# Kernel tuning notes

Measured on AMD Instinct MI355X. Metric: run time of the kernel, lower is better.

## Reference

```python
import jax, jax.numpy as jnp
import numpy as np
from jax import lax

B, CIN, H, W = 32, 256, 56, 56
COUT, M, K = 256, 2, 3
CMID = COUT * M  # 512
SPARSITY = 0.9


def _make_binary_weight(key):
    k1, k2 = jax.random.split(key)
    shape = (CMID, CIN, K, K)
    mask = jax.random.bernoulli(k1, SPARSITY, shape)
    sign = jax.random.bernoulli(k2, 0.5, shape).astype(jnp.float32) * 2.0 - 1.0
    return jnp.where(mask, sign, 0.0).astype(jnp.float32)


def setup_inputs() -> dict:
    key = jax.random.key(0)
    kx, kw, kfw, kfb = jax.random.split(key, 4)
    x = jax.random.normal(kx, (B, CIN, H, W), dtype=jnp.float32)
    binary_w = _make_binary_weight(kw)
    fan_in = CMID  # 1x1 conv fan-in
    bound = 1.0 / np.sqrt(fan_in)
    fc_w = jax.random.uniform(kfw, (COUT, CMID, 1, 1), minval=-bound, maxval=bound, dtype=jnp.float32)
    fc_b = jax.random.uniform(kfb, (COUT,), minval=-bound, maxval=bound, dtype=jnp.float32)
    return {"x": x, "binary_w": binary_w, "fc_w": fc_w, "fc_b": fc_b}


def reference(x, binary_w, fc_w, fc_b):
    pad = K // 2
    # fixed random ternary conv, stride 1, same padding
    y = lax.conv_general_dilated(
        x, binary_w, window_strides=(1, 1), padding=[(pad, pad), (pad, pad)],
        dimension_numbers=("NCHW", "OIHW", "NCHW"))
    y = jax.nn.relu(y)
    # learnable 1x1 conv with bias
    y = lax.conv_general_dilated(
        y, fc_w, window_strides=(1, 1), padding=[(0, 0), (0, 0)],
        dimension_numbers=("NCHW", "OIHW", "NCHW"))
    return y + fc_b[None, :, None, None]
```

## Files before the change

kernel.cpp:

```cpp
#include <hip/hip_runtime.h>
#include <hip/hip_bf16.h>
#include <stdint.h>


typedef __attribute__((ext_vector_type(8))) short short8;
typedef __attribute__((ext_vector_type(4))) float floatx4;

#define ROWE 8192
#define NT_PER_B 28

#define OFF_WP  0
#define OFF_A2  2359296
#define OFF_XP  2621440
#define OFF_Y   63439872

__device__ static inline void async16(const void* gptr, void* lptr) {
  __builtin_amdgcn_global_load_lds(
      (const __attribute__((address_space(1))) void*)gptr,
      (__attribute__((address_space(3))) void*)lptr,
      16, 0, 0);
}

__device__ static inline unsigned short f2bf(float x) {
  __hip_bfloat16 h = __float2bfloat16(x);
  return *reinterpret_cast<unsigned short*>(&h);
}

__global__ void k_xprep(const float* __restrict__ x, __hip_bfloat16* __restrict__ Xp) {
  const int t = blockIdx.x * 256 + threadIdx.x;
  const int wq  = t & 63;
  const int khi = (t >> 6) & 15;
  const int t2  = t >> 10;
  const int hp  = t2 % 58;
  const int bc  = t2 / 58;
  const int b   = bc >> 1;
  const int cin0 = ((bc & 1) << 7) + (khi << 3);
  const int h = hp - 1, w = wq - 1;
  unsigned short v[8];
  if ((unsigned)h < 56u && (unsigned)w < 56u) {
    const float* xp = x + ((size_t)(b * 256 + cin0) * 56 + h) * 56 + w;
#pragma unroll
    for (int j = 0; j < 8; ++j) v[j] = f2bf(xp[(size_t)j * 3136]);
  } else {
#pragma unroll
    for (int j = 0; j < 8; ++j) v[j] = 0;
  }
  uint4 pk;
  pk.x = (unsigned)v[0] | ((unsigned)v[1] << 16);
  pk.y = (unsigned)v[2] | ((unsigned)v[3] << 16);
  pk.z = (unsigned)v[4] | ((unsigned)v[5] << 16);
  pk.w = (unsigned)v[6] | ((unsigned)v[7] << 16);
  *(uint4*)(Xp + (size_t)t * 8) = pk;
}

__global__ void k_wprep(const float* __restrict__ bw, __hip_bfloat16* __restrict__ Wp) {
  const int idx = blockIdx.x * 256 + threadIdx.x;
  const int klo = idx & 7;
  const int cml = (idx >> 3) & 63;
  const int khi = (idx >> 9) & 15;
  const int cmh = (idx >> 13) & 1;
  const int rest = idx >> 14;
  const int cmblk = rest & 3;
  const int tcg = rest >> 2;
  const int cg  = tcg & 1;
  const int tap = tcg >> 1;
  const int kh = tap / 3, kw = tap - kh * 3;
  const int cm  = (cmblk << 7) + (cmh << 6) + cml;
  const int cin = (cg << 7) + (khi << 3) + klo;
  Wp[idx] = __float2bfloat16(bw[((cm * 256 + cin) * 3 + kh) * 3 + kw]);
}

__global__ void k_a2prep(const float* __restrict__ fw, __hip_bfloat16* __restrict__ A2) {
  const int idx = blockIdx.x * 256 + threadIdx.x;
  const int klo = idx & 7;
  const int cl  = (idx >> 3) & 63;
  const int khi = (idx >> 9) & 15;
  const int ch  = (idx >> 13) & 1;
  const int rest = idx >> 14;
  const int mtile = rest & 1;
  const int cg = rest >> 1;
  const int cout = (mtile << 7) + (ch << 6) + cl;
  const int cm   = (cg << 7) + (khi << 3) + klo;
  A2[idx] = __float2bfloat16(fw[cout * 512 + cm]);
}

__global__ __launch_bounds__(256, 2) void k_conv1(
    const __hip_bfloat16* __restrict__ Xp, const __hip_bfloat16* __restrict__ Wp,
    __hip_bfloat16* __restrict__ Y) {
  __shared__ short8 lds_raw[4096];
  char* lds = (char*)lds_raw;
  const int tid  = threadIdx.x;
  const int lane = tid & 63;
  const int wv   = tid >> 6;
  const int wm   = wv >> 1, wn = wv & 1;
  const int l15  = lane & 15;
  const int quad = lane >> 4;
  const int id   = blockIdx.x;
  const int xcd  = id & 7;
  const int seq  = id >> 3;
  const int cmblk = seq & 3;
  const int ntile = xcd * 112 + (seq >> 2);
  const int b  = ntile / NT_PER_B;
  const int h0 = (ntile % NT_PER_B) * 2;

  floatx4 acc[4][4];
#pragma unroll
  for (int i = 0; i < 4; i++)
#pragma unroll
    for (int j = 0; j < 4; j++) acc[i][j] = (floatx4){0.f, 0.f, 0.f, 0.f};

  for (int t = 0; t < 18; ++t) {
    const int tap = t >> 1;
    const int cg  = t & 1;
    const int kh = tap / 3, kw = tap - kh * 3;
    const size_t a_base = (size_t)((tap * 2 + cg) * 4 + cmblk) * 16384;
    const size_t b_base = (size_t)((b * 2 + cg) * 58 + (h0 + kh)) * ROWE + kw * 8;
    __syncthreads();
    const char* gA = (const char*)(Wp + a_base) + wv * 8192 + lane * 16;
    const char* gB = (const char*)(Xp + b_base) + wv * 8192 + lane * 16;
    char* lA = lds + wv * 8192;
    char* lB = lds + 32768 + wv * 8192;
#pragma unroll
    for (int c = 0; c < 8; ++c) {
      async16(gA + c * 1024, lA + c * 1024);
      async16(gB + c * 1024, lB + c * 1024);
    }
    __syncthreads();
#pragma unroll
    for (int kk = 0; kk < 4; ++kk) {
      short8 af[4], bf[4];
#pragma unroll
      for (int mi = 0; mi < 4; ++mi) {
        const int m = wm * 64 + mi * 16 + l15;
        af[mi] = *(const short8*)(lds + ((m >> 6) * 16 + kk * 4 + quad) * 1024 + (m & 63) * 16);
      }
#pragma unroll
      for (int ni = 0; ni < 4; ++ni) {
        const int n = wn * 64 + ni * 16 + l15;
        bf[ni] = *(const short8*)(lds + 32768 + ((n >> 6) * 16 + kk * 4 + quad) * 1024 + (n & 63) * 16);
      }
#pragma unroll
      for (int mi = 0; mi < 4; ++mi)
#pragma unroll
        for (int ni = 0; ni < 4; ++ni)
          acc[mi][ni] = __builtin_amdgcn_mfma_f32_16x16x32_bf16(af[mi], bf[ni], acc[mi][ni], 0, 0, 0);
    }
  }

  const size_t ybase = ((size_t)ntile * 4 + cmblk) * 16384;
#pragma unroll
  for (int mi = 0; mi < 4; ++mi) {
    const int cml  = wm * 64 + mi * 16 + quad * 4;
    const int khi  = cml >> 3;
    const int klo0 = cml & 7;
#pragma unroll
    for (int ni = 0; ni < 4; ++ni) {
      const int n = wn * 64 + ni * 16 + l15;
      const int r = n >> 6, w = n & 63;
      floatx4 f = acc[mi][ni];
      unsigned lo = (unsigned)f2bf(fmaxf(f[0], 0.f)) | ((unsigned)f2bf(fmaxf(f[1], 0.f)) << 16);
      unsigned hi = (unsigned)f2bf(fmaxf(f[2], 0.f)) | ((unsigned)f2bf(fmaxf(f[3], 0.f)) << 16);
      uint2 pk = make_uint2(lo, hi);
      *(uint2*)((char*)Y + (ybase + (size_t)r * 8192 + khi * 512 + w * 8 + klo0) * 2) = pk;
    }
  }
}

__global__ __launch_bounds__(256, 2) void k_conv2(
    const __hip_bfloat16* __restrict__ Y, const __hip_bfloat16* __restrict__ A2,
    const float* __restrict__ fcb, float* __restrict__ out) {
  __shared__ short8 lds_raw[4096];
  char* lds = (char*)lds_raw;
  const int tid  = threadIdx.x;
  const int lane = tid & 63;
  const int wv   = tid >> 6;
  const int wm   = wv >> 1, wn = wv & 1;
  const int l15  = lane & 15;
  const int quad = lane >> 4;
  const int id   = blockIdx.x;
  const int xcd  = id & 7;
  const int seq  = id >> 3;
  const int mtile = seq & 1;
  const int rp    = xcd * 112 + (seq >> 1);

  floatx4 acc[4][4];
#pragma unroll
  for (int i = 0; i < 4; i++)
#pragma unroll
    for (int j = 0; j < 4; j++) acc[i][j] = (floatx4){0.f, 0.f, 0.f, 0.f};

  for (int cg = 0; cg < 4; ++cg) {
    const size_t a_base = (size_t)(cg * 2 + mtile) * 16384;
    const size_t b_base = (size_t)(rp * 4 + cg) * 16384;
    __syncthreads();
    const char* gA = (const char*)(A2 + a_base) + wv * 8192 + lane * 16;
    const char* gB = (const char*)(Y + b_base) + wv * 8192 + lane * 16;
    char* lA = lds + wv * 8192;
    char* lB = lds + 32768 + wv * 8192;
#pragma unroll
    for (int c = 0; c < 8; ++c) {
      async16(gA + c * 1024, lA + c * 1024);
      async16(gB + c * 1024, lB + c * 1024);
    }
    __syncthreads();
#pragma unroll
    for (int kk = 0; kk < 4; ++kk) {
      short8 af[4], bf[4];
#pragma unroll
      for (int mi = 0; mi < 4; ++mi) {
        const int m = wm * 64 + mi * 16 + l15;
        af[mi] = *(const short8*)(lds + ((m >> 6) * 16 + kk * 4 + quad) * 1024 + (m & 63) * 16);
      }
#pragma unroll
      for (int ni = 0; ni < 4; ++ni) {
        const int n = wn * 64 + ni * 16 + l15;
        bf[ni] = *(const short8*)(lds + 32768 + ((n >> 6) * 16 + kk * 4 + quad) * 1024 + (n & 63) * 16);
      }
#pragma unroll
      for (int mi = 0; mi < 4; ++mi)
#pragma unroll
        for (int ni = 0; ni < 4; ++ni)
          acc[mi][ni] = __builtin_amdgcn_mfma_f32_16x16x32_bf16(af[mi], bf[ni], acc[mi][ni], 0, 0, 0);
    }
  }

  const int b   = rp / NT_PER_B;
  const int nb0 = (rp % NT_PER_B) * 128;
#pragma unroll
  for (int mi = 0; mi < 4; ++mi) {
    const int co = mtile * 128 + wm * 64 + mi * 16 + quad * 4;
#pragma unroll
    for (int ni = 0; ni < 4; ++ni) {
      const int n = wn * 64 + ni * 16 + l15;
      const int w = n & 63;
      if (w < 56) {
        const int nb = nb0 + n;
        const int h  = nb >> 6;
        floatx4 f = acc[mi][ni];
        const size_t base = (size_t)(b * 256 + co) * 3136 + h * 56 + w;
#pragma unroll
        for (int r = 0; r < 4; ++r)
          out[base + (size_t)r * 3136] = f[r] + fcb[co + r];
      }
    }
  }
}

extern "C" void kernel_launch(void* const* d_in, const int* in_sizes, int n_in,
                              void* d_out, int out_size, void* d_ws, size_t ws_size,
                              hipStream_t stream) {
  const float* x  = (const float*)d_in[0];
  const float* bw = (const float*)d_in[1];
  const float* fw = (const float*)d_in[2];
  const float* fb = (const float*)d_in[3];
  float* out = (float*)d_out;
  char* ws = (char*)d_ws;

  __hip_bfloat16* Wp = (__hip_bfloat16*)(ws + OFF_WP);
  __hip_bfloat16* A2 = (__hip_bfloat16*)(ws + OFF_A2);
  __hip_bfloat16* Xp = (__hip_bfloat16*)(ws + OFF_XP);
  __hip_bfloat16* Y  = (__hip_bfloat16*)(ws + OFF_Y);

  k_wprep<<<dim3(4608), dim3(256), 0, stream>>>(bw, Wp);
  k_a2prep<<<dim3(512), dim3(256), 0, stream>>>(fw, A2);
  k_xprep<<<dim3(14848), dim3(256), 0, stream>>>(x, Xp);
  k_conv1<<<dim3(3584), dim3(256), 0, stream>>>(Xp, Wp, Y);
  k_conv2<<<dim3(1792), dim3(256), 0, stream>>>(Y, A2, fb, out);
}
```

Measured before the change: 474.3 us.

## Halve K-chunk per stage to 64 and raise occupancy to five blocks per CU

Measured after the change: 479.9 us. About the same (+1.2%).

```diff
diff --git a/kernel.cpp b/kernel.cpp
--- a/kernel.cpp
+++ b/kernel.cpp
@@ -6,7 +6,6 @@
 typedef __attribute__((ext_vector_type(8))) short short8;
 typedef __attribute__((ext_vector_type(4))) float floatx4;
 
-#define ROWE 8192
 #define NT_PER_B 28
 
 #define OFF_WP  0
@@ -55,40 +54,36 @@
 
 __global__ void k_wprep(const float* __restrict__ bw, __hip_bfloat16* __restrict__ Wp) {
   const int idx = blockIdx.x * 256 + threadIdx.x;
-  const int klo = idx & 7;
-  const int cml = (idx >> 3) & 63;
-  const int khi = (idx >> 9) & 15;
-  const int cmh = (idx >> 13) & 1;
-  const int rest = idx >> 14;
-  const int cmblk = rest & 3;
-  const int tcg = rest >> 2;
-  const int cg  = tcg & 1;
-  const int tap = tcg >> 1;
-  const int kh = tap / 3, kw = tap - kh * 3;
+  const int klo   = idx & 7;
+  const int cml   = (idx >> 3) & 63;
+  const int khi   = (idx >> 9) & 7;
+  const int cmh   = (idx >> 12) & 1;
+  const int khalf = (idx >> 13) & 1;
+  const int cmblk = (idx >> 14) & 3;
+  const int cg    = (idx >> 16) & 1;
+  const int tap   = idx >> 17;
   const int cm  = (cmblk << 7) + (cmh << 6) + cml;
-  const int cin = (cg << 7) + (khi << 3) + klo;
-  Wp[idx] = __float2bfloat16(bw[((cm * 256 + cin) * 3 + kh) * 3 + kw]);
+  const int cin = (cg << 7) + (khalf << 6) + (khi << 3) + klo;
+  Wp[idx] = __float2bfloat16(bw[(cm * 256 + cin) * 9 + tap]);
 }
 
 __global__ void k_a2prep(const float* __restrict__ fw, __hip_bfloat16* __restrict__ A2) {
   const int idx = blockIdx.x * 256 + threadIdx.x;
-  const int klo = idx & 7;
-  const int cl  = (idx >> 3) & 63;
-  const int khi = (idx >> 9) & 15;
-  const int ch  = (idx >> 13) & 1;
-  const int rest = idx >> 14;
-  const int mtile = rest & 1;
-  const int cg = rest >> 1;
+  const int klo   = idx & 7;
+  const int cl    = (idx >> 3) & 63;
+  const int khi   = (idx >> 9) & 7;
+  const int ch    = (idx >> 12) & 1;
+  const int mtile = (idx >> 13) & 1;
+  const int kblk  = idx >> 14;
   const int cout = (mtile << 7) + (ch << 6) + cl;
-  const int cm   = (cg << 7) + (khi << 3) + klo;
+  const int cm   = (kblk << 6) + (khi << 3) + klo;
   A2[idx] = __float2bfloat16(fw[cout * 512 + cm]);
 }
 
-__global__ __launch_bounds__(256, 2) void k_conv1(
+__global__ __launch_bounds__(256, 5) void k_conv1(
     const __hip_bfloat16* __restrict__ Xp, const __hip_bfloat16* __restrict__ Wp,
     __hip_bfloat16* __restrict__ Y) {
-  __shared__ short8 lds_raw[4096];
-  char* lds = (char*)lds_raw;
+  __shared__ char lds[32768];
   const int tid  = threadIdx.x;
   const int lane = tid & 63;
   const int wv   = tid >> 6;
@@ -102,6 +97,8 @@
   const int ntile = xcd * 112 + (seq >> 2);
   const int b  = ntile / NT_PER_B;
   const int h0 = (ntile % NT_PER_B) * 2;
+  const char* WpB = (const char*)Wp;
+  const char* XpB = (const char*)Xp;
 
   floatx4 acc[4][4];
 #pragma unroll
@@ -109,35 +106,35 @@
 #pragma unroll
     for (int j = 0; j < 4; j++) acc[i][j] = (floatx4){0.f, 0.f, 0.f, 0.f};
 
-  for (int t = 0; t < 18; ++t) {
-    const int tap = t >> 1;
-    const int cg  = t & 1;
+  for (int t = 0; t < 36; ++t) {
+    const int tap   = t >> 2;
+    const int cg    = (t >> 1) & 1;
+    const int khalf = t & 1;
     const int kh = tap / 3, kw = tap - kh * 3;
-    const size_t a_base = (size_t)((tap * 2 + cg) * 4 + cmblk) * 16384;
-    const size_t b_base = (size_t)((b * 2 + cg) * 58 + (h0 + kh)) * ROWE + kw * 8;
-    __syncthreads();
-    const char* gA = (const char*)(Wp + a_base) + wv * 8192 + lane * 16;
-    const char* gB = (const char*)(Xp + b_base) + wv * 8192 + lane * 16;
-    char* lA = lds + wv * 8192;
-    char* lB = lds + 32768 + wv * 8192;
-#pragma unroll
-    for (int c = 0; c < 8; ++c) {
-      async16(gA + c * 1024, lA + c * 1024);
-      async16(gB + c * 1024, lB + c * 1024);
-    }
-    __syncthreads();
-#pragma unroll
-    for (int kk = 0; kk < 4; ++kk) {
+    const size_t a_base = (size_t)((((tap * 2 + cg) * 4 + cmblk) * 2) + khalf) << 14;
+    const size_t b_base = ((size_t)((b * 2 + cg) * 58 + (h0 + kh)) << 14) + kw * 16 + (khalf << 13);
+    __syncthreads();
+#pragma unroll
+    for (int c = 0; c < 4; ++c) {
+      const int off = c * 4096 + tid * 16;
+      async16(WpB + a_base + off, lds + off);
+      const int row = off >> 13;
+      const int inner = off & 8191;
+      async16(XpB + b_base + (size_t)row * 16384 + inner, lds + 16384 + off);
+    }
+    __syncthreads();
+#pragma unroll
+    for (int kk = 0; kk < 2; ++kk) {
       short8 af[4], bf[4];
 #pragma unroll
       for (int mi = 0; mi < 4; ++mi) {
         const int m = wm * 64 + mi * 16 + l15;
-        af[mi] = *(const short8*)(lds + ((m >> 6) * 16 + kk * 4 + quad) * 1024 + (m & 63) * 16);
+        af[mi] = *(const short8*)(lds + (m >> 6) * 8192 + (kk * 4 + quad) * 1024 + (m & 63) * 16);
       }
 #pragma unroll
       for (int ni = 0; ni < 4; ++ni) {
         const int n = wn * 64 + ni * 16 + l15;
-        bf[ni] = *(const short8*)(lds + 32768 + ((n >> 6) * 16 + kk * 4 + quad) * 1024 + (n & 63) * 16);
+        bf[ni] = *(const short8*)(lds + 16384 + (n >> 6) * 8192 + (kk * 4 + quad) * 1024 + (n & 63) * 16);
       }
 #pragma unroll
       for (int mi = 0; mi < 4; ++mi)
@@ -150,9 +147,10 @@
   const size_t ybase = ((size_t)ntile * 4 + cmblk) * 16384;
 #pragma unroll
   for (int mi = 0; mi < 4; ++mi) {
-    const int cml  = wm * 64 + mi * 16 + quad * 4;
-    const int khi  = cml >> 3;
-    const int klo0 = cml & 7;
+    const int cmL   = wm * 64 + mi * 16 + quad * 4;
+    const int khalf = (cmL >> 6) & 1;
+    const int khi   = (cmL >> 3) & 7;
+    const int klo0  = cmL & 7;
 #pragma unroll
     for (int ni = 0; ni < 4; ++ni) {
       const int n = wn * 64 + ni * 16 + l15;
@@ -161,16 +159,15 @@
       unsigned lo = (unsigned)f2bf(fmaxf(f[0], 0.f)) | ((unsigned)f2bf(fmaxf(f[1], 0.f)) << 16);
       unsigned hi = (unsigned)f2bf(fmaxf(f[2], 0.f)) | ((unsigned)f2bf(fmaxf(f[3], 0.f)) << 16);
       uint2 pk = make_uint2(lo, hi);
-      *(uint2*)((char*)Y + (ybase + (size_t)r * 8192 + khi * 512 + w * 8 + klo0) * 2) = pk;
-    }
-  }
-}
-
-__global__ __launch_bounds__(256, 2) void k_conv2(
+      *(uint2*)((char*)Y + (ybase + (size_t)khalf * 8192 + r * 4096 + khi * 512 + w * 8 + klo0) * 2) = pk;
+    }
+  }
+}
+
+__global__ __launch_bounds__(256, 5) void k_conv2(
     const __hip_bfloat16* __restrict__ Y, const __hip_bfloat16* __restrict__ A2,
     const float* __restrict__ fcb, float* __restrict__ out) {
-  __shared__ short8 lds_raw[4096];
-  char* lds = (char*)lds_raw;
+  __shared__ char lds[32768];
   const int tid  = threadIdx.x;
   const int lane = tid & 63;
   const int wv   = tid >> 6;
@@ -182,6 +179,8 @@
   const int seq  = id >> 3;
   const int mtile = seq & 1;
   const int rp    = xcd * 112 + (seq >> 1);
+  const char* A2B = (const char*)A2;
+  const char* YB  = (const char*)Y;
 
   floatx4 acc[4][4];
 #pragma unroll
@@ -189,32 +188,29 @@
 #pragma unroll
     for (int j = 0; j < 4; j++) acc[i][j] = (floatx4){0.f, 0.f, 0.f, 0.f};
 
-  for (int cg = 0; cg < 4; ++cg) {
-    const size_t a_base = (size_t)(cg * 2 + mtile) * 16384;
-    const size_t b_base = (size_t)(rp * 4 + cg) * 16384;
-    __syncthreads();
-    const char* gA = (const char*)(A2 + a_base) + wv * 8192 + lane * 16;
-    const char* gB = (const char*)(Y + b_base) + wv * 8192 + lane * 16;
-    char* lA = lds + wv * 8192;
-    char* lB = lds + 32768 + wv * 8192;
-#pragma unroll
-    for (int c = 0; c < 8; ++c) {
-      async16(gA + c * 1024, lA + c * 1024);
-      async16(gB + c * 1024, lB + c * 1024);
-    }
-    __syncthreads();
-#pragma unroll
-    for (int kk = 0; kk < 4; ++kk) {
+  for (int kb = 0; kb < 8; ++kb) {
+    const size_t a_base = (size_t)(kb * 2 + mtile) << 14;
+    const size_t b_base = ((size_t)(rp * 4 + (kb >> 1)) << 15) + ((size_t)(kb & 1) << 14);
+    __syncthreads();
+#pragma unroll
+    for (int c = 0; c < 4; ++c) {
+      const int off = c * 4096 + tid * 16;
+      async16(A2B + a_base + off, lds + off);
+      async16(YB + b_base + off, lds + 16384 + off);
+    }
+    __syncthreads();
+#pragma unroll
+    for (int kk = 0; kk < 2; ++kk) {
       short8 af[4], bf[4];
 #pragma unroll
       for (int mi = 0; mi < 4; ++mi) {
         const int m = wm * 64 + mi * 16 + l15;
-        af[mi] = *(const short8*)(lds + ((m >> 6) * 16 + kk * 4 + quad) * 1024 + (m & 63) * 16);
+        af[mi] = *(const short8*)(lds + (m >> 6) * 8192 + (kk * 4 + quad) * 1024 + (m & 63) * 16);
       }
 #pragma unroll
       for (int ni = 0; ni < 4; ++ni) {
         const int n = wn * 64 + ni * 16 + l15;
-        bf[ni] = *(const short8*)(lds + 32768 + ((n >> 6) * 16 + kk * 4 + quad) * 1024 + (n & 63) * 16);
+        bf[ni] = *(const short8*)(lds + 16384 + (n >> 6) * 8192 + (kk * 4 + quad) * 1024 + (n & 63) * 16);
       }
 #pragma unroll
       for (int mi = 0; mi < 4; ++mi)
```
